# Performance work log

Hardware: AMD Instinct MI355X
Metric: run time of the kernel (lower is better)

Reference implementation:

```python
import jax, jax.numpy as jnp
import numpy as np

B, T, C, H = 4, 2048, 512, 8
HS = C // H  # head_size = 64
EPS = 1e-5


def layernorm(x, g, b):
    mu = jnp.mean(x, axis=-1, keepdims=True)
    var = jnp.mean(jnp.square(x - mu), axis=-1, keepdims=True)
    return (x - mu) * jax.lax.rsqrt(var + EPS) * g + b


def setup_inputs() -> dict:
    key = jax.random.key(0)
    ks = jax.random.split(key, 12)
    s_attn = 1.0 / np.sqrt(C)
    s_ff1 = 1.0 / np.sqrt(C)
    s_ff2 = 1.0 / np.sqrt(4 * C)
    return {
        "x": jax.random.normal(ks[0], (B, T, C), jnp.float32),
        "wq": jax.random.normal(ks[1], (H, C, HS), jnp.float32) * s_attn,
        "wk": jax.random.normal(ks[2], (H, C, HS), jnp.float32) * s_attn,
        "wv": jax.random.normal(ks[3], (H, C, HS), jnp.float32) * s_attn,
        "w1": jax.random.normal(ks[4], (C, 4 * C), jnp.float32) * s_ff1,
        "b1": jnp.zeros((4 * C,), jnp.float32),
        "w2": jax.random.normal(ks[5], (4 * C, C), jnp.float32) * s_ff2,
        "b2": jnp.zeros((C,), jnp.float32),
        "ln1_g": jnp.ones((C,), jnp.float32),
        "ln1_b": jnp.zeros((C,), jnp.float32),
        "ln2_g": jnp.ones((C,), jnp.float32),
        "ln2_b": jnp.zeros((C,), jnp.float32),
    }


def reference(x, wq, wk, wv, w1, b1, w2, b2, ln1_g, ln1_b, ln2_g, ln2_b):
    # pre-LN multi-head causal self-attention
    h = layernorm(x, ln1_g, ln1_b)                       # [B,T,C]
    q = jnp.einsum("btc,hcd->bhtd", h, wq)
    k = jnp.einsum("btc,hcd->bhtd", h, wk)
    v = jnp.einsum("btc,hcd->bhtd", h, wv)
    # NOTE: source scales by full embed dim C, not head_size
    scores = jnp.einsum("bhtd,bhsd->bhts", q, k) * (C ** -0.5)  # [B,H,T,T]
    causal = jnp.tril(jnp.ones((T, T), bool))
    scores = jnp.where(causal, scores, -jnp.inf)
    att = jax.nn.softmax(scores, axis=-1)
    out = jnp.einsum("bhts,bhsd->bhtd", att, v)          # [B,H,T,HS]
    out = out.transpose(0, 2, 1, 3).reshape(B, T, C)     # concat heads
    x = x + out
    # FFN with residual
    h2 = layernorm(x, ln2_g, ln2_b)
    ff = jax.nn.relu(h2 @ w1 + b1) @ w2 + b2
    return x + ff
```

## Files before the change

kernel.cpp:

```cpp
#include <hip/hip_runtime.h>

typedef unsigned short ushort_t;
typedef __attribute__((ext_vector_type(8))) short short8;
typedef __attribute__((ext_vector_type(4))) float floatx4;

#define B_  4
#define T_  2048
#define C_  512
#define H_  8
#define HS_ 64
#define M_  (B_*T_)
#define SCALE2 0.06376140168547404f

__device__ __forceinline__ float b2f(ushort_t u) {
  union { unsigned int i; float f; } w; w.i = ((unsigned int)u) << 16; return w.f;
}
__device__ __forceinline__ ushort_t f2b(float f) {
  union { float f; unsigned int i; } w; w.f = f;
  unsigned int x = w.i;
  return (ushort_t)((x + 0x7fffu + ((x >> 16) & 1u)) >> 16);
}
__device__ __forceinline__ unsigned int cvtpk(float a, float b) {
  unsigned int r;
  asm("v_cvt_pk_bf16_f32 %0, %1, %2" : "=v"(r) : "v"(a), "v"(b));
  return r;
}
__device__ __forceinline__ void gl_lds16(const ushort_t* g, ushort_t* l) {
  __builtin_amdgcn_global_load_lds((const unsigned int*)g, (unsigned int*)l, 16, 0, 0);
}

__global__ __launch_bounds__(256) void transpose_all(const float* __restrict__ wq,
                                                     const float* __restrict__ wk,
                                                     const float* __restrict__ wv,
                                                     const float* __restrict__ w1,
                                                     const float* __restrict__ w2,
                                                     ushort_t* __restrict__ qkvt,
                                                     ushort_t* __restrict__ w1t,
                                                     ushort_t* __restrict__ w2t) {
  __shared__ ushort_t t[32][33];
  int idx = blockIdx.x;
  const float* in; ushort_t* out; int K, N, bx, by, z = 0;
  float scl = (idx < 256) ? SCALE2 : 1.0f;
  if (idx < 768) {
    int seg = idx >> 8, li = idx & 255;
    in = seg == 0 ? wq : (seg == 1 ? wk : wv);
    out = qkvt + (size_t)seg * 262144;
    K = 512; N = 64;
    z = li >> 5; li &= 31;
    bx = li & 1; by = li >> 1;
  } else if (idx < 1792) {
    int li = idx - 768;
    in = w1; out = w1t; K = 512; N = 2048;
    bx = li & 63; by = li >> 6;
  } else {
    int li = idx - 1792;
    in = w2; out = w2t; K = 2048; N = 512;
    bx = li & 15; by = li >> 4;
  }
  size_t zoff = (size_t)z * K * N;
  int n0 = bx * 32, k0 = by * 32;
  int tx = threadIdx.x & 31, ty = threadIdx.x >> 5;
#pragma unroll
  for (int i = 0; i < 4; i++)
    t[ty + 8 * i][tx] = f2b(in[zoff + (size_t)(k0 + ty + 8 * i) * N + n0 + tx] * scl);
  __syncthreads();
#pragma unroll
  for (int i = 0; i < 4; i++)
    out[zoff + (size_t)(n0 + ty + 8 * i) * K + k0 + tx] = t[tx][ty + 8 * i];
}

__global__ __launch_bounds__(256) void ln_k(const float* __restrict__ X,
                                            const float* __restrict__ g,
                                            const float* __restrict__ bb,
                                            ushort_t* __restrict__ Y) {
  int wave = threadIdx.x >> 6, lane = threadIdx.x & 63;
  size_t row = (size_t)blockIdx.x * 4 + wave;
  float v[8], s = 0.f, s2 = 0.f;
#pragma unroll
  for (int i = 0; i < 8; i++) {
    float x = X[row * C_ + lane + 64 * i];
    v[i] = x; s += x; s2 += x * x;
  }
#pragma unroll
  for (int off = 32; off >= 1; off >>= 1) {
    s += __shfl_xor(s, off); s2 += __shfl_xor(s2, off);
  }
  float mu = s * (1.0f / C_);
  float var = s2 * (1.0f / C_) - mu * mu;
  float rs = rsqrtf(var + 1e-5f);
  ushort_t* yr = Y + row * C_;
#pragma unroll
  for (int i = 0; i < 8; i++) {
    int c = lane + 64 * i;
    yr[c] = f2b((v[i] - mu) * rs * g[c] + bb[c]);
  }
}

__global__ __launch_bounds__(256) void gemm_bt128(const ushort_t* __restrict__ A,
                                                  const ushort_t* __restrict__ Bt,
                                                  ushort_t* __restrict__ Out,
                                                  int K, int ldOut,
                                                  const float* __restrict__ bias,
                                                  int relu) {
  __shared__ __align__(16) ushort_t As[128 * 64];
  __shared__ __align__(16) ushort_t Bs[128 * 64];
  const int tid = threadIdx.x;
  const int lane = tid & 63, wave = tid >> 6;
  const long row0 = (long)blockIdx.x * 128;
  const long col0 = (long)blockIdx.y * 128;
  const int srow = wave * 32 + (lane >> 3);
  const int scol = (((lane & 7) ^ ((lane >> 3) & 7))) * 8;
  const ushort_t* Ab = A + (size_t)(row0 + srow) * K + scol;
  const ushort_t* Bb = Bt + (size_t)(col0 + srow) * K + scol;
  const int wm = (wave >> 1) * 64, wn = (wave & 1) * 64;
  const int fq = lane >> 4, fl = lane & 15;
  floatx4 acc[4][4] = {};

  for (int k0 = 0; k0 < K; k0 += 64) {
    __syncthreads();
#pragma unroll
    for (int i = 0; i < 4; i++) {
      gl_lds16(Ab + (size_t)(i * 8) * K + k0, &As[(wave * 32 + i * 8) * 64]);
      gl_lds16(Bb + (size_t)(i * 8) * K + k0, &Bs[(wave * 32 + i * 8) * 64]);
    }
    __syncthreads();
#pragma unroll
    for (int ks = 0; ks < 2; ks++) {
      short8 af[4], bf[4];
      const int sl = ((ks * 4 + fq) ^ (fl & 7)) * 8;
#pragma unroll
      for (int i = 0; i < 4; i++) {
        af[i] = *(const short8*)&As[(wm + i * 16 + fl) * 64 + sl];
        bf[i] = *(const short8*)&Bs[(wn + i * 16 + fl) * 64 + sl];
      }
#pragma unroll
      for (int fi = 0; fi < 4; fi++)
#pragma unroll
        for (int fj = 0; fj < 4; fj++)
          acc[fi][fj] = __builtin_amdgcn_mfma_f32_16x16x32_bf16(af[fi], bf[fj], acc[fi][fj], 0, 0, 0);
    }
  }
#pragma unroll
  for (int fi = 0; fi < 4; fi++)
#pragma unroll
    for (int fj = 0; fj < 4; fj++) {
      long gcol = col0 + wn + fj * 16 + fl;
      float bv = bias ? bias[gcol] : 0.0f;
#pragma unroll
      for (int r = 0; r < 4; r++) {
        long grow = row0 + wm + fi * 16 + fq * 4 + r;
        float v = acc[fi][fj][r] + bv;
        if (relu) v = fmaxf(v, 0.0f);
        Out[(size_t)grow * ldOut + gcol] = f2b(v);
      }
    }
}

__global__ __launch_bounds__(256) void gemm_bt64(const ushort_t* __restrict__ A,
                                                 const ushort_t* __restrict__ Bt,
                                                 float* __restrict__ Out,
                                                 int K, int ldOut,
                                                 const float* __restrict__ bias,
                                                 const float* __restrict__ residual) {
  __shared__ __align__(16) ushort_t As[64 * 64];
  __shared__ __align__(16) ushort_t Bs[64 * 64];
  const int tid = threadIdx.x;
  const int lane = tid & 63, wave = tid >> 6;
  const long row0 = (long)blockIdx.x * 64;
  const long col0 = (long)blockIdx.y * 64;
  const int srow = wave * 16 + (lane >> 3);
  const int scol = (((lane & 7) ^ ((lane >> 3) & 7))) * 8;
  const ushort_t* Ab = A + (size_t)(row0 + srow) * K + scol;
  const ushort_t* Bb = Bt + (size_t)(col0 + srow) * K + scol;
  const int wm = (wave >> 1) * 32, wn = (wave & 1) * 32;
  const int fq = lane >> 4, fl = lane & 15;
  floatx4 acc[2][2] = {};

  for (int k0 = 0; k0 < K; k0 += 64) {
    __syncthreads();
#pragma unroll
    for (int i = 0; i < 2; i++) {
      gl_lds16(Ab + (size_t)(i * 8) * K + k0, &As[(wave * 16 + i * 8) * 64]);
      gl_lds16(Bb + (size_t)(i * 8) * K + k0, &Bs[(wave * 16 + i * 8) * 64]);
    }
    __syncthreads();
#pragma unroll
    for (int ks = 0; ks < 2; ks++) {
      short8 af[2], bf[2];
      const int sl = ((ks * 4 + fq) ^ (fl & 7)) * 8;
#pragma unroll
      for (int i = 0; i < 2; i++) {
        af[i] = *(const short8*)&As[(wm + i * 16 + fl) * 64 + sl];
        bf[i] = *(const short8*)&Bs[(wn + i * 16 + fl) * 64 + sl];
      }
#pragma unroll
      for (int fi = 0; fi < 2; fi++)
#pragma unroll
        for (int fj = 0; fj < 2; fj++)
          acc[fi][fj] = __builtin_amdgcn_mfma_f32_16x16x32_bf16(af[fi], bf[fj], acc[fi][fj], 0, 0, 0);
    }
  }
#pragma unroll
  for (int fi = 0; fi < 2; fi++)
#pragma unroll
    for (int fj = 0; fj < 2; fj++) {
      long gcol = col0 + wn + fj * 16 + fl;
      float bv = bias[gcol];
#pragma unroll
      for (int r = 0; r < 4; r++) {
        long grow = row0 + wm + fi * 16 + fq * 4 + r;
        size_t oi = (size_t)grow * ldOut + gcol;
        Out[oi] = acc[fi][fj][r] + bv + residual[oi];
      }
    }
}

__global__ __launch_bounds__(256) void flash_attn(const ushort_t* __restrict__ QKV,
                                                  const float* __restrict__ X,
                                                  float* __restrict__ X1) {
  __shared__ __align__(16) ushort_t kt[2][64 * 72];
  __shared__ __align__(16) ushort_t vt[2][64 * 72];
  const int tid = threadIdx.x;
  const int lane = tid & 63, wave = tid >> 6;
  const int fq = lane >> 4, fl = lane & 15;
  const int g = blockIdx.x >> 5;
  const int tile = g < 16 ? 31 - g : g - 16;
  const int bh = blockIdx.x & 31;
  const int h = bh & 7, b = bh >> 3;
  const int hoff = h * HS_;
  const int q0 = tile * 64;
  const int LD = 3 * C_;
  const int nst = tile + 1;
  const int qg = q0 + wave * 16 + fl;

  short8 qf0, qf1;
  {
    const ushort_t* qp = QKV + (size_t)((size_t)b * T_ + q0 + wave * 16 + fl) * LD + hoff + fq * 8;
    qf0 = *(const short8*)(qp);
    qf1 = *(const short8*)(qp + 32);
  }
  short8 of;
  {
    short ob = (fl == 0) ? (short)0x3F80 : (short)0;
#pragma unroll
    for (int i = 0; i < 8; i++) of[i] = ob;
  }
  floatx4 oacc[4] = {};
  floatx4 lacc = {};

  const int role = tid >> 7;
  const int t2 = tid & 127;
  const int sr4 = (t2 >> 3) * 4;
  const int d0 = (t2 & 7) * 8;
  const ushort_t* sbase = QKV + (size_t)((size_t)b * T_ + sr4) * LD + hoff +
                          (role ? C_ : 2 * C_);

  const int addrA = ((2 * (fq & 1)) * 16 + fl) * 4;
  const int addrB = addrA + 64;
  const bool lowq = fq < 2;

  short8 r0 = *(const short8*)(sbase + d0);
  short8 r1 = *(const short8*)(sbase + LD + d0);
  short8 r2 = *(const short8*)(sbase + 2 * LD + d0);
  short8 r3 = *(const short8*)(sbase + 3 * LD + d0);
  if (role) {
    *(short8*)&kt[0][sr4 * 72 + d0] = r0;
    *(short8*)&kt[0][(sr4 + 1) * 72 + d0] = r1;
    *(short8*)&kt[0][(sr4 + 2) * 72 + d0] = r2;
    *(short8*)&kt[0][(sr4 + 3) * 72 + d0] = r3;
  } else {
#pragma unroll
    for (int i = 0; i < 8; i++) {
      int d = d0 + i;
      int scol = sr4 ^ (8 * (d >> 3));
      unsigned int pkA = ((unsigned int)(ushort_t)r0[i]) |
                         (((unsigned int)(ushort_t)r1[i]) << 16);
      unsigned int pkB = ((unsigned int)(ushort_t)r2[i]) |
                         (((unsigned int)(ushort_t)r3[i]) << 16);
      *(unsigned int*)&vt[0][d * 72 + scol] = pkA;
      *(unsigned int*)&vt[0][d * 72 + scol + 2] = pkB;
    }
  }
  {
    const ushort_t* sp = sbase + (size_t)64 * LD;
    r0 = *(const short8*)(sp + d0);
    r1 = *(const short8*)(sp + LD + d0);
    r2 = *(const short8*)(sp + 2 * LD + d0);
    r3 = *(const short8*)(sp + 3 * LD + d0);
  }

  for (int st = 0; st < nst; st++) {
    __syncthreads();
    const int cur = st & 1;
    if (st + 1 < nst) {
      const int nb = cur ^ 1;
      if (role) {
        *(short8*)&kt[nb][sr4 * 72 + d0] = r0;
        *(short8*)&kt[nb][(sr4 + 1) * 72 + d0] = r1;
        *(short8*)&kt[nb][(sr4 + 2) * 72 + d0] = r2;
        *(short8*)&kt[nb][(sr4 + 3) * 72 + d0] = r3;
      } else {
#pragma unroll
        for (int i = 0; i < 8; i++) {
          int d = d0 + i;
          int scol = sr4 ^ (8 * (d >> 3));
          unsigned int pkA = ((unsigned int)(ushort_t)r0[i]) |
                             (((unsigned int)(ushort_t)r1[i]) << 16);
          unsigned int pkB = ((unsigned int)(ushort_t)r2[i]) |
                             (((unsigned int)(ushort_t)r3[i]) << 16);
          *(unsigned int*)&vt[nb][d * 72 + scol] = pkA;
          *(unsigned int*)&vt[nb][d * 72 + scol + 2] = pkB;
        }
      }
      if (st + 2 < nst) {
        const ushort_t* sp = sbase + (size_t)(st + 2) * 64 * LD;
        r0 = *(const short8*)(sp + d0);
        r1 = *(const short8*)(sp + LD + d0);
        r2 = *(const short8*)(sp + 2 * LD + d0);
        r3 = *(const short8*)(sp + 3 * LD + d0);
      }
    }

    {
      const int s0 = st * 64;
      floatx4 sacc[4] = {};
#pragma unroll
      for (int fn = 0; fn < 4; fn++) {
        short8 kf0 = *(const short8*)&kt[cur][(fn * 16 + fl) * 72 + fq * 8];
        short8 kf1 = *(const short8*)&kt[cur][(fn * 16 + fl) * 72 + 32 + fq * 8];
        sacc[fn] = __builtin_amdgcn_mfma_f32_16x16x32_bf16(kf0, qf0, sacc[fn], 0, 0, 0);
        sacc[fn] = __builtin_amdgcn_mfma_f32_16x16x32_bf16(kf1, qf1, sacc[fn], 0, 0, 0);
      }
      const bool diag = (st == tile);
      unsigned int xc[4][2];
#pragma unroll
      for (int fn = 0; fn < 4; fn++) {
        float p[4];
#pragma unroll
        for (int r = 0; r < 4; r++) {
          float pv = exp2f(sacc[fn][r]);
          if (diag && (s0 + fn * 16 + fq * 4 + r) > qg) pv = 0.0f;
          p[r] = pv;
        }
        xc[fn][0] = cvtpk(p[0], p[1]);
        xc[fn][1] = cvtpk(p[2], p[3]);
      }
      union U8 { unsigned int u[4]; short8 s8; } pu[2];
#pragma unroll
      for (int o = 0; o < 2; o++)
#pragma unroll
        for (int t = 0; t < 4; t++) {
          int ad = (t >> 1) ? addrB : addrA;
          int lo = __builtin_amdgcn_ds_bpermute(ad, (int)xc[2 * o][t & 1]);
          int hi = __builtin_amdgcn_ds_bpermute(ad, (int)xc[2 * o + 1][t & 1]);
          pu[o].u[t] = lowq ? (unsigned int)lo : (unsigned int)hi;
        }
      short8 pf0 = pu[0].s8, pf1 = pu[1].s8;
#pragma unroll
      for (int fn = 0; fn < 4; fn++) {
        int drow = fn * 16 + fl;
        int sw = 8 * (drow >> 3);
        short8 vf0 = *(const short8*)&vt[cur][drow * 72 + ((fq * 8) ^ sw)];
        short8 vf1 = *(const short8*)&vt[cur][drow * 72 + ((32 + fq * 8) ^ sw)];
        oacc[fn] = __builtin_amdgcn_mfma_f32_16x16x32_bf16(pf0, vf0, oacc[fn], 0, 0, 0);
        oacc[fn] = __builtin_amdgcn_mfma_f32_16x16x32_bf16(pf1, vf1, oacc[fn], 0, 0, 0);
      }
      lacc = __builtin_amdgcn_mfma_f32_16x16x32_bf16(pf0, of, lacc, 0, 0, 0);
      lacc = __builtin_amdgcn_mfma_f32_16x16x32_bf16(pf1, of, lacc, 0, 0, 0);
    }
  }
#pragma unroll
  for (int r = 0; r < 4; r++) {
    float lr = __shfl(lacc[r], lane & 48);
    float inv = 1.0f / lr;
    int qgr = q0 + wave * 16 + fq * 4 + r;
#pragma unroll
    for (int fn = 0; fn < 4; fn++) {
      int d = fn * 16 + fl;
      size_t oi = ((size_t)b * T_ + qgr) * C_ + hoff + d;
      X1[oi] = oacc[fn][r] * inv + X[oi];
    }
  }
}

extern "C" void kernel_launch(void* const* d_in, const int* in_sizes, int n_in,
                              void* d_out, int out_size, void* d_ws, size_t ws_size,
                              hipStream_t stream) {
  const float* x  = (const float*)d_in[0];
  const float* wq = (const float*)d_in[1];
  const float* wk = (const float*)d_in[2];
  const float* wv = (const float*)d_in[3];
  const float* w1 = (const float*)d_in[4];
  const float* b1 = (const float*)d_in[5];
  const float* w2 = (const float*)d_in[6];
  const float* b2 = (const float*)d_in[7];
  const float* ln1g = (const float*)d_in[8];
  const float* ln1b = (const float*)d_in[9];
  const float* ln2g = (const float*)d_in[10];
  const float* ln2b = (const float*)d_in[11];
  ushort_t* ws = (ushort_t*)d_ws;

  const size_t SZ = (size_t)M_ * C_;
  ushort_t* qkvt = ws;
  ushort_t* w1t  = qkvt + 786432;
  ushort_t* w2t  = w1t + 1048576;
  ushort_t* qkv  = w2t + 1048576;
  ushort_t* h2   = qkv;
  ushort_t* ff1  = qkv + SZ;
  ushort_t* h    = (ushort_t*)d_out;
  float* x1      = (float*)d_out;
  float* outf    = (float*)d_out;

  transpose_all<<<2816, 256, 0, stream>>>(wq, wk, wv, w1, w2, qkvt, w1t, w2t);
  ln_k<<<M_ / 4, 256, 0, stream>>>(x, ln1g, ln1b, h);
  gemm_bt128<<<dim3(64, 12), 256, 0, stream>>>(h, qkvt, qkv, 512, 1536, nullptr, 0);
  flash_attn<<<B_ * H_ * (T_ / 64), 256, 0, stream>>>(qkv, x, x1);
  ln_k<<<M_ / 4, 256, 0, stream>>>(x1, ln2g, ln2b, h2);
  for (int p = 0; p < 2; p++) {
    const size_t roff = (size_t)p * 4096;
    gemm_bt128<<<dim3(32, 16), 256, 0, stream>>>(h2 + roff * C_, w1t, ff1,
                                                 512, 2048, b1, 1);
    gemm_bt64<<<dim3(64, 8), 256, 0, stream>>>(ff1, w2t, outf + roff * C_,
                                               2048, 512, b2, x1 + roff * C_);
  }
}
```

Before: 245.5 us.

## Run FFN unsplit with a 128x128-tile down-projection GEMM when workspace allows

When the workspace is large enough, the FFN runs as one up-projection over all 8192 rows instead of two halves. The down-projection now uses a new 128x128-tile bf16 MFMA kernel that adds bias and residual and writes fp32 output, replacing the 64x64-tile kernel. This cuts kernel launches and raises per-block data reuse in the K=2048 GEMM. The cost is fewer blocks (256) for the down-projection, plus a larger workspace requirement. If the workspace is too small, the old split path still runs.

Result: faster. 239.7 us (-2.4%).

```diff
diff --git a/kernel.cpp b/kernel.cpp
--- a/kernel.cpp
+++ b/kernel.cpp
@@ -156,6 +156,65 @@
     }
 }
 
+__global__ __launch_bounds__(256) void gemm_bt128_f32(const ushort_t* __restrict__ A,
+                                                      const ushort_t* __restrict__ Bt,
+                                                      float* __restrict__ Out,
+                                                      int K, int ldOut,
+                                                      const float* __restrict__ bias,
+                                                      const float* __restrict__ residual) {
+  __shared__ __align__(16) ushort_t As[128 * 64];
+  __shared__ __align__(16) ushort_t Bs[128 * 64];
+  const int tid = threadIdx.x;
+  const int lane = tid & 63, wave = tid >> 6;
+  const long row0 = (long)blockIdx.x * 128;
+  const long col0 = (long)blockIdx.y * 128;
+  const int srow = wave * 32 + (lane >> 3);
+  const int scol = (((lane & 7) ^ ((lane >> 3) & 7))) * 8;
+  const ushort_t* Ab = A + (size_t)(row0 + srow) * K + scol;
+  const ushort_t* Bb = Bt + (size_t)(col0 + srow) * K + scol;
+  const int wm = (wave >> 1) * 64, wn = (wave & 1) * 64;
+  const int fq = lane >> 4, fl = lane & 15;
+  floatx4 acc[4][4] = {};
+
+  for (int k0 = 0; k0 < K; k0 += 64) {
+    __syncthreads();
+#pragma unroll
+    for (int i = 0; i < 4; i++) {
+      gl_lds16(Ab + (size_t)(i * 8) * K + k0, &As[(wave * 32 + i * 8) * 64]);
+      gl_lds16(Bb + (size_t)(i * 8) * K + k0, &Bs[(wave * 32 + i * 8) * 64]);
+    }
+    __syncthreads();
+#pragma unroll
+    for (int ks = 0; ks < 2; ks++) {
+      short8 af[4], bf[4];
+      const int sl = ((ks * 4 + fq) ^ (fl & 7)) * 8;
+#pragma unroll
+      for (int i = 0; i < 4; i++) {
+        af[i] = *(const short8*)&As[(wm + i * 16 + fl) * 64 + sl];
+        bf[i] = *(const short8*)&Bs[(wn + i * 16 + fl) * 64 + sl];
+      }
+#pragma unroll
+      for (int fi = 0; fi < 4; fi++)
+#pragma unroll
+        for (int fj = 0; fj < 4; fj++)
+          acc[fi][fj] = __builtin_amdgcn_mfma_f32_16x16x32_bf16(af[fi], bf[fj], acc[fi][fj], 0, 0, 0);
+    }
+  }
+#pragma unroll
+  for (int fi = 0; fi < 4; fi++)
+#pragma unroll
+    for (int fj = 0; fj < 4; fj++) {
+      long gcol = col0 + wn + fj * 16 + fl;
+      float bv = bias[gcol];
+#pragma unroll
+      for (int r = 0; r < 4; r++) {
+        long grow = row0 + wm + fi * 16 + fq * 4 + r;
+        size_t oi = (size_t)grow * ldOut + gcol;
+        Out[oi] = acc[fi][fj][r] + bv + residual[oi];
+      }
+    }
+}
+
 __global__ __launch_bounds__(256) void gemm_bt64(const ushort_t* __restrict__ A,
                                                  const ushort_t* __restrict__ Bt,
                                                  float* __restrict__ Out,
@@ -411,16 +470,24 @@
   float* x1      = (float*)d_out;
   float* outf    = (float*)d_out;
 
+  const size_t need_unsplit = (2883584 + 5 * SZ) * sizeof(ushort_t);
+
   transpose_all<<<2816, 256, 0, stream>>>(wq, wk, wv, w1, w2, qkvt, w1t, w2t);
   ln_k<<<M_ / 4, 256, 0, stream>>>(x, ln1g, ln1b, h);
   gemm_bt128<<<dim3(64, 12), 256, 0, stream>>>(h, qkvt, qkv, 512, 1536, nullptr, 0);
   flash_attn<<<B_ * H_ * (T_ / 64), 256, 0, stream>>>(qkv, x, x1);
   ln_k<<<M_ / 4, 256, 0, stream>>>(x1, ln2g, ln2b, h2);
-  for (int p = 0; p < 2; p++) {
-    const size_t roff = (size_t)p * 4096;
-    gemm_bt128<<<dim3(32, 16), 256, 0, stream>>>(h2 + roff * C_, w1t, ff1,
-                                                 512, 2048, b1, 1);
-    gemm_bt64<<<dim3(64, 8), 256, 0, stream>>>(ff1, w2t, outf + roff * C_,
-                                               2048, 512, b2, x1 + roff * C_);
-  }
-}
+  if (ws_size >= need_unsplit) {
+    gemm_bt128<<<dim3(64, 16), 256, 0, stream>>>(h2, w1t, ff1, 512, 2048, b1, 1);
+    gemm_bt128_f32<<<dim3(64, 4), 256, 0, stream>>>(ff1, w2t, outf, 2048, 512,
+                                                    b2, x1);
+  } else {
+    for (int p = 0; p < 2; p++) {
+      const size_t roff = (size_t)p * 4096;
+      gemm_bt128<<<dim3(32, 16), 256, 0, stream>>>(h2 + roff * C_, w1t, ff1,
+                                                   512, 2048, b1, 1);
+      gemm_bt64<<<dim3(64, 8), 256, 0, stream>>>(ff1, w2t, outf + roff * C_,
+                                                 2048, 512, b2, x1 + roff * C_);
+    }
+  }
+}
```
